# Kernel tuning notes

Hardware: AMD Instinct MI355X
Metric: run time of the kernel (lower is better)

The kernel has to match this reference:

```python
import jax, jax.numpy as jnp
import numpy as np

B, L, D, C, NL = 32, 512, 768, 97, 2  # batch, seq_len, hidden, class_nums, gat_layers


def setup_inputs() -> dict:
    key = jax.random.key(0)
    ks = jax.random.split(key, 16)

    def n(k, shape, scale=0.02):
        return jax.random.normal(k, shape, dtype=jnp.float32) * scale

    return dict(
        x=n(ks[0], (B, L, D), 1.0),                 # encoder output
        pos1=jnp.ones((B, L), jnp.float32),          # entity-1 position mask
        pos2=jnp.ones((B, L), jnp.float32),          # entity-2 position mask
        mask=jnp.ones((B, L), jnp.int32),            # attention mask (1 = keep)
        emb=n(ks[1], (C, D), 1.0),                   # relation label embedding table
        rel_w=n(ks[2], (D, D)), rel_b=jnp.zeros((D,), jnp.float32),
        # per-layer, per-RA (axis1: 0=ra1, 1=ra2) parameters
        qw=n(ks[3], (NL, 2, D, D)), qb=jnp.zeros((NL, 2, D), jnp.float32),
        kw=n(ks[4], (NL, 2, D, D)), kb=jnp.zeros((NL, 2, D), jnp.float32),
        vw=n(ks[5], (NL, 2, D, D)), vb=jnp.zeros((NL, 2, D), jnp.float32),
        sw=n(ks[6], (NL, 2, 2 * D)), sb=jnp.zeros((NL, 2), jnp.float32),   # score: Linear(2d,1)
        gw=n(ks[7], (NL, 2, 2 * D)), gb=jnp.zeros((NL, 2), jnp.float32),   # gate:  Linear(2d,1)
        fc1_w=n(ks[8], (3 * D, D)), fc1_b=jnp.zeros((D,), jnp.float32),
        fc2_w=n(ks[9], (D,)), fc2_b=jnp.zeros((), jnp.float32),
    )


def _relation_attention(p, x, qw, qb, kw, kb, vw, vb, sw, sb, gw, gb, mask):
    # p: (b, c, d) queries; x: (b, l, d) keys/values
    d = p.shape[-1]
    q = jnp.einsum('bcd,de->bce', p, qw) + qb          # (b, c, d)
    k = jnp.einsum('bld,de->ble', x, kw) + kb          # (b, l, d)
    # score = Linear(concat([q_i, k_j])) is separable: q@sw[:d] + k@sw[d:] + sb
    score = (q @ sw[:d])[:, :, None] + (k @ sw[d:])[:, None, :] + sb  # (b, c, l)
    if mask is not None:
        score = jnp.where(mask[:, None, :] == 0, jnp.float32(-1e9), score)
    attn = jax.nn.softmax(score, axis=2)
    v = jnp.einsum('bld,de->ble', x, vw) + vb          # (b, l, d)
    out = jnp.einsum('bcl,bld->bcd', attn, v) + p      # (b, c, d)
    # gate = sigmoid(Linear(concat([out, p]))), also separable
    g = jax.nn.sigmoid(out @ gw[:d] + p @ gw[d:] + gb)[..., None]
    return g * out + (1.0 - g) * p


def reference(x, pos1, pos2, mask, emb, rel_w, rel_b,
              qw, qb, kw, kb, vw, vb, sw, sb, gw, gb,
              fc1_w, fc1_b, fc2_w, fc2_b):
    b, d = x.shape[0], x.shape[-1]
    # p = relation(embedding(arange(C))) broadcast over batch
    p = emb @ rel_w + rel_b                            # (C, d)
    p = jnp.broadcast_to(p[None], (b,) + p.shape)      # (b, C, d)

    for li in range(qw.shape[0]):
        x = _relation_attention(x, p, qw[li, 0], qb[li, 0], kw[li, 0], kb[li, 0],
                                vw[li, 0], vb[li, 0], sw[li, 0], sb[li, 0],
                                gw[li, 0], gb[li, 0], None) + x
        p = _relation_attention(p, x, qw[li, 1], qb[li, 1], kw[li, 1], kb[li, 1],
                                vw[li, 1], vb[li, 1], sw[li, 1], sb[li, 1],
                                gw[li, 1], gb[li, 1], mask) + p

    def pool_avg(pos):
        return jnp.sum(x * pos[:, :, None], axis=1) / jnp.sum(pos, axis=1)[:, None]

    e1 = pool_avg(pos1)                                # (b, d)
    e2 = pool_avg(pos2)                                # (b, d)
    cshape = p.shape                                   # (b, C, d)
    pc = jnp.concatenate([p,
                          jnp.broadcast_to(e1[:, None, :], cshape),
                          jnp.broadcast_to(e2[:, None, :], cshape)], axis=2)  # (b, C, 3d)
    h = jnp.tanh(pc @ fc1_w + fc1_b)                   # (b, C, d)
    logits = jax.nn.sigmoid(h @ fc2_w + fc2_b)         # (b, C)
    pred = jnp.argmax(logits, axis=1)                  # (b,)
    return logits, pred
```

## Files before the change

### kernel.cpp

```cpp
#include <hip/hip_runtime.h>
#include <math.h>

#define NBLK 512
#define NTHR 256
static const int Bb = 32, Ls = 512, Dd = 768, Cc = 97;

struct KArgs {
    const float *x0, *pos1, *pos2;
    const int* mask;
    const float *emb, *rel_w, *rel_b, *kw, *vw, *vb, *sw, *gw, *gb;
    const float *fc1w, *fc1b, *fc2w, *fc2b;
    float* out;
    float *p0b, *pp, *sc, *avx1, *avx2, *av1, *av2, *aw1, *aw2, *S0, *S1, *xp1, *xp2, *geb;
    float *kvecs, *pdots, *g1buf, *xd;
    float* zbase;
    int zcount;
};

__device__ __forceinline__ float sigm(float x) { return 1.f / (1.f + expf(-x)); }

__device__ __forceinline__ float wred(float v) {
#pragma unroll
    for (int o = 32; o > 0; o >>= 1) v += __shfl_down(v, o, 64);
    return v;
}

__device__ __forceinline__ float blk_sum4(float v, float* shr) {
    v = wred(v);
    int t = threadIdx.x;
    if ((t & 63) == 0) shr[t >> 6] = v;
    __syncthreads();
    float r = shr[0] + shr[1] + shr[2] + shr[3];
    __syncthreads();
    return r;
}

__device__ void sgemm_direct(const float* __restrict__ A, const float* __restrict__ W,
                             const float* __restrict__ bias, float* __restrict__ C,
                             int M, int N, int K, int bx, int by,
                             float* As, float* Ws) {
    int tid = threadIdx.x;
    int tx = tid & 15, ty = tid >> 4;
    int bn = bx * 64, bm = by * 64;
    int arow = tid >> 2, akq = (tid & 3) << 2;
    int wrow = tid >> 4, wcol = (tid & 15) << 2;
    int gar = bm + arow;
    bool aval = gar < M;
    const float* Ap = A + (size_t)gar * K + akq;
    const float* Wp = W + (size_t)wrow * N + bn + wcol;
    float acc[4][4] = {{0.f}};
    float4 a4 = make_float4(0.f, 0.f, 0.f, 0.f);
    if (aval) a4 = *(const float4*)Ap;
    float4 w4 = *(const float4*)Wp;
    for (int k0 = 0; k0 < K; k0 += 16) {
        __syncthreads();
        As[(akq + 0) * 64 + arow] = a4.x; As[(akq + 1) * 64 + arow] = a4.y;
        As[(akq + 2) * 64 + arow] = a4.z; As[(akq + 3) * 64 + arow] = a4.w;
        *(float4*)&Ws[wrow * 64 + wcol] = w4;
        __syncthreads();
        if (k0 + 16 < K) {
            if (aval) a4 = *(const float4*)(Ap + k0 + 16);
            w4 = *(const float4*)(Wp + (size_t)(k0 + 16) * N);
        }
#pragma unroll
        for (int kk = 0; kk < 16; ++kk) {
            float4 a = *(const float4*)&As[kk * 64 + (ty << 2)];
            float4 b = *(const float4*)&Ws[kk * 64 + (tx << 2)];
            acc[0][0]+=a.x*b.x; acc[0][1]+=a.x*b.y; acc[0][2]+=a.x*b.z; acc[0][3]+=a.x*b.w;
            acc[1][0]+=a.y*b.x; acc[1][1]+=a.y*b.y; acc[1][2]+=a.y*b.z; acc[1][3]+=a.y*b.w;
            acc[2][0]+=a.z*b.x; acc[2][1]+=a.z*b.y; acc[2][2]+=a.z*b.z; acc[2][3]+=a.z*b.w;
            acc[3][0]+=a.w*b.x; acc[3][1]+=a.w*b.y; acc[3][2]+=a.w*b.z; acc[3][3]+=a.w*b.w;
        }
    }
    int gc = bn + (tx << 2);
    float4 bz4 = make_float4(0.f, 0.f, 0.f, 0.f);
    if (bias) bz4 = *(const float4*)(bias + gc);
#pragma unroll
    for (int i = 0; i < 4; ++i) {
        int gr = bm + (ty << 2) + i;
        if (gr < M) {
            float4 o = make_float4(acc[i][0] + bz4.x, acc[i][1] + bz4.y,
                                   acc[i][2] + bz4.z, acc[i][3] + bz4.w);
            *(float4*)(C + (size_t)gr * N + gc) = o;
        }
    }
}

__device__ void sm_w(const KArgs& a, int phase, int b, float* shr,
                     float& w0o, float& w1o, float& ga0, float& ga1,
                     float& gb0o, float& gb1o) {
    int t = threadIdx.x;
    float ks[2], ga[2], gb2[2] = {0.f, 0.f};
#pragma unroll
    for (int i = 0; i < 2; ++i) {
        int l = t + (i << 8);
        size_t r = (size_t)b * Ls + l;
        const float* px = a.xd + r * 4;
        float gp = sigm(px[0] + a.sc[b] + a.gb[0]);
        if (phase == 0) {
            ga[i] = gp;
            ks[i] = 2.f * px[1] + gp * a.sc[32 + b];
        } else {
            float g = sigm(2.f * px[2] + gp * a.sc[64 + b] + a.sc[224 + b] + a.gb[2]);
            ga[i] = gp; gb2[i] = g;
            ks[i] = 4.f * px[3] + 2.f * gp * a.sc[96 + b] + g * a.sc[256 + b];
        }
        if (a.mask[r] == 0) ks[i] = -1e9f;
    }
    float mx = fmaxf(ks[0], ks[1]);
#pragma unroll
    for (int o = 32; o > 0; o >>= 1) mx = fmaxf(mx, __shfl_down(mx, o, 64));
    if ((t & 63) == 0) shr[t >> 6] = mx;
    __syncthreads();
    mx = fmaxf(fmaxf(shr[0], shr[1]), fmaxf(shr[2], shr[3]));
    __syncthreads();
    float e0 = expf(ks[0] - mx), e1 = expf(ks[1] - mx);
    float s = blk_sum4(e0 + e1, shr);
    float inv = 1.f / s;
    w0o = e0 * inv; w1o = e1 * inv;
    ga0 = ga[0]; ga1 = ga[1];
    gb0o = gb2[0]; gb1o = gb2[1];
}

__device__ void coeff0_dev(const KArgs& a, int b, float* shr) {
    float w0, w1, ga0, ga1, u0, u1;
    sm_w(a, 0, b, shr, w0, w1, ga0, ga1, u0, u1);
    float ca = blk_sum4(w0 * ga0 + w1 * ga1, shr);
    if (threadIdx.x == 0) a.sc[320 + b] = ca;
}

__device__ void coeff1_dev(const KArgs& a, int b, float* shr) {
    int t = threadIdx.x;
    float w0, w1, ga0, ga1, g0, g1;
    sm_w(a, 1, b, shr, w0, w1, ga0, ga1, g0, g1);
    float ca = blk_sum4(w0 * ga0 + w1 * ga1, shr);
    if (t == 0) a.sc[352 + b] = ca;
    float cb = blk_sum4(w0 * g0 + w1 * g1, shr);
    if (t == 0) a.sc[384 + b] = cb;
    float q1a = a.pos1[(size_t)b * Ls + t], q1b = a.pos1[(size_t)b * Ls + t + 256];
    float q2a = a.pos2[(size_t)b * Ls + t], q2b = a.pos2[(size_t)b * Ls + t + 256];
    float s1 = blk_sum4(q1a + q1b, shr);
    float s2 = blk_sum4(q2a + q2b, shr);
    float c11 = blk_sum4(q1a * ga0 + q1b * ga1, shr);
    float c12 = blk_sum4(q1a * g0 + q1b * g1, shr);
    float c21 = blk_sum4(q2a * ga0 + q2b * ga1, shr);
    float c22 = blk_sum4(q2a * g0 + q2b * g1, shr);
    if (t == 0) {
        a.sc[448 + b] = c11; a.sc[480 + b] = c12;
        a.sc[512 + b] = c21; a.sc[544 + b] = c22;
        a.sc[576 + b] = 1.f / s1; a.sc[608 + b] = 1.f / s2;
    }
}

__device__ void attn_gemv(const KArgs& a, int phase, int jlin,
                          float* xs, float* lw, float* shr) {
    int t = threadIdx.x;
    int jt = jlin % 3, b = (jlin / 3) % 32, kseg = jlin / 96;
    float v = -3.0e38f, g1 = 0.f;
    if (t < Cc) {
        if (phase == 0) v = a.pdots[t];
        else {
            g1 = sigm(a.pdots[194 + t] + a.sc[128 + b] + a.gb[1]);
            v = 2.f * a.pdots[97 + t] + g1 * a.sc[160 + b];
        }
    }
    if (phase == 1 && jt == 0 && kseg == 0 && t < Cc) a.g1buf[(size_t)b * Cc + t] = g1;
    float m = v;
#pragma unroll
    for (int o = 32; o > 0; o >>= 1) m = fmaxf(m, __shfl_down(m, o, 64));
    if ((t & 63) == 0) shr[t >> 6] = m;
    __syncthreads();
    m = fmaxf(fmaxf(shr[0], shr[1]), fmaxf(shr[2], shr[3]));
    __syncthreads();
    float e = (t < Cc) ? expf(v - m) : 0.f;
    float s = blk_sum4(e, shr);
    float wc = e / s;
    if (t < Cc) lw[t] = wc;
    float cg1 = blk_sum4(wc * g1, shr);
    float alpha = (phase == 0) ? 1.f : 2.f;
    if (t < 96) {
        int d = kseg * 96 + t;
        const float* pc = a.p0b + d;
        float acc2 = 0.f;
#pragma unroll 4
        for (int c = 0; c < Cc; ++c) acc2 += lw[c] * pc[(size_t)c * Dd];
        float val = alpha * acc2;
        if (phase == 1) val += cg1 * a.av1[(size_t)b * Dd + d];
        xs[t] = val;
    }
    __syncthreads();
    const float* W = a.vw + (size_t)(phase == 0 ? 0 : 2) * Dd * Dd;
    const float* bias = a.vb + (phase == 0 ? 0 : 2) * Dd;
    float* outp = (phase == 0) ? a.avx1 : a.avx2;
    int j = jt * 256 + t;
    float acc = (kseg == 0) ? bias[j] : 0.f;
    const float* wp = W + (size_t)(kseg * 96) * Dd + j;
#pragma unroll 8
    for (int dd = 0; dd < 96; ++dd) acc += xs[dd] * wp[(size_t)dd * Dd];
    atomicAdd(&outp[(size_t)b * Dd + j], acc);
    const float* da[4]; const float* db[4]; int nd; float* dout;
    if (phase == 0) {
        da[0]=a.gw;          db[0]=nullptr;
        da[1]=a.kvecs+Dd;    db[1]=nullptr;
        da[2]=a.gw+3072;     db[2]=a.gw+3840;
        da[3]=a.kvecs+3*Dd;  db[3]=nullptr;
        nd = 4; dout = a.sc;
    } else {
        da[0]=a.gw+3072;     db[0]=nullptr;
        da[1]=a.kvecs+3*Dd;  db[1]=nullptr;
        nd = 2; dout = a.sc + 224;
    }
    for (int vv = 0; vv < nd; ++vv) {
        float wv = da[vv][j] + (db[vv] ? db[vv][j] : 0.f);
        float p = blk_sum4(acc * wv, shr);
        if (t == 0) atomicAdd(&dout[vv * 32 + b], p);
    }
    __syncthreads();
}

__device__ void mm_dev(const KArgs& a, int jlin, const float* S, float gamma,
                       const float* avA, const float* coefA, float multA,
                       const float* avB, const float* coefB, float multB,
                       const float* W, const float* bias, float* outp,
                       int ndots, const float* d0a, const float* d0b,
                       const float* d1a, const float* d2a, const float* d2b,
                       float* dout, float* xs, float* shr) {
    int t = threadIdx.x;
    int jt = jlin % 3, b = (jlin / 3) % 32, kseg = jlin / 96;
    if (t < 96) {
        int d = kseg * 96 + t;
        float v = gamma * S[(size_t)b * Dd + d];
        if (avA) v += multA * coefA[b] * avA[(size_t)b * Dd + d];
        if (avB) v += multB * coefB[b] * avB[(size_t)b * Dd + d];
        xs[t] = v;
    }
    __syncthreads();
    int j = jt * 256 + t;
    float acc = (kseg == 0 && bias) ? bias[j] : 0.f;
    const float* wp = W + (size_t)(kseg * 96) * Dd + j;
#pragma unroll 8
    for (int dd = 0; dd < 96; ++dd) acc += xs[dd] * wp[(size_t)dd * Dd];
    atomicAdd(&outp[(size_t)b * Dd + j], acc);
    if (ndots > 0) {
        float wv = d0a[j] + (d0b ? d0b[j] : 0.f);
        float p = blk_sum4(acc * wv, shr);
        if (t == 0) atomicAdd(&dout[b], p);
    }
    if (ndots > 1) {
        float p = blk_sum4(acc * d1a[j], shr);
        if (t == 0) atomicAdd(&dout[32 + b], p);
    }
    if (ndots > 2) {
        float wv = d2a[j] + (d2b ? d2b[j] : 0.f);
        float p = blk_sum4(acc * wv, shr);
        if (t == 0) atomicAdd(&dout[64 + b], p);
    }
}

__device__ void ge_dev(const KArgs& a, int jlin, float* xs, float* xs2) {
    int t = threadIdx.x;
    int jt = jlin % 3, b = (jlin / 3) % 32, kseg = jlin / 96;
    if (t < 96) {
        int d = kseg * 96 + t;
        float a1 = a.avx1[(size_t)b * Dd + d], a2 = a.avx2[(size_t)b * Dd + d];
        xs[t]  = (4.f * a.xp1[(size_t)b * Dd + d] + 2.f * a.sc[448 + b] * a1
                  + a.sc[480 + b] * a2) * a.sc[576 + b];
        xs2[t] = (4.f * a.xp2[(size_t)b * Dd + d] + 2.f * a.sc[512 + b] * a1
                  + a.sc[544 + b] * a2) * a.sc[608 + b];
    }
    __syncthreads();
    int j = jt * 256 + t;
    float a1 = 0.f, a2 = 0.f;
    const float* w1 = a.fc1w + (size_t)(Dd + kseg * 96) * Dd + j;
    const float* w2 = a.fc1w + (size_t)(2 * Dd + kseg * 96) * Dd + j;
#pragma unroll 8
    for (int dd = 0; dd < 96; ++dd) {
        a1 += xs[dd] * w1[(size_t)dd * Dd];
        a2 += xs2[dd] * w2[(size_t)dd * Dd];
    }
    float res = a1 + a2 + (kseg == 0 ? a.fc1b[j] : 0.f);
    atomicAdd(&a.geb[(size_t)b * Dd + j], res);
}

__device__ void aw_one(const KArgs& a, int jlin, const float* av, float* outp, float* xs) {
    int t = threadIdx.x;
    int jt = jlin % 3, b = (jlin / 3) % 32, kseg = jlin / 96;
    if (t < 96) xs[t] = av[(size_t)b * Dd + kseg * 96 + t];
    __syncthreads();
    int j = jt * 256 + t;
    float acc = 0.f;
    const float* wp = a.fc1w + (size_t)(kseg * 96) * Dd + j;
#pragma unroll 8
    for (int dd = 0; dd < 96; ++dd) acc += xs[dd] * wp[(size_t)dd * Dd];
    atomicAdd(&outp[(size_t)b * Dd + j], acc);
}

__device__ void passX_dev(const KArgs& a, int phase, int blk, float* S, bool dopos,
                          float* smw, float* shr) {
    int t = threadIdx.x;
    int b = blk >> 4, seg = blk & 15, l0 = seg * 32;
    {
        float w0, w1, u0, u1, u2, u3;
        sm_w(a, phase, b, shr, w0, w1, u0, u1, u2, u3);
        smw[t] = w0; smw[t + 256] = w1;
    }
    __syncthreads();
    if (t < 192) {
        int d4 = t << 2;
        const float* xb = a.x0 + ((size_t)b * Ls + l0) * Dd + d4;
        float4 as = make_float4(0.f,0.f,0.f,0.f);
        float4 a1 = make_float4(0.f,0.f,0.f,0.f);
        float4 a2 = make_float4(0.f,0.f,0.f,0.f);
        for (int l = 0; l < 32; ++l) {
            float4 xv = *(const float4*)(xb + (size_t)l * Dd);
            float wv = smw[l0 + l];
            as.x += wv*xv.x; as.y += wv*xv.y; as.z += wv*xv.z; as.w += wv*xv.w;
            if (dopos) {
                float q1 = a.pos1[(size_t)b * Ls + l0 + l], q2 = a.pos2[(size_t)b * Ls + l0 + l];
                a1.x += q1*xv.x; a1.y += q1*xv.y; a1.z += q1*xv.z; a1.w += q1*xv.w;
                a2.x += q2*xv.x; a2.y += q2*xv.y; a2.z += q2*xv.z; a2.w += q2*xv.w;
            }
        }
        float* ds = S + (size_t)b * Dd + d4;
        atomicAdd(ds+0, as.x); atomicAdd(ds+1, as.y); atomicAdd(ds+2, as.z); atomicAdd(ds+3, as.w);
        if (dopos) {
            float* d1 = a.xp1 + (size_t)b * Dd + d4;
            float* d2 = a.xp2 + (size_t)b * Dd + d4;
            atomicAdd(d1+0, a1.x); atomicAdd(d1+1, a1.y); atomicAdd(d1+2, a1.z); atomicAdd(d1+3, a1.w);
            atomicAdd(d2+0, a2.x); atomicAdd(d2+1, a2.y); atomicAdd(d2+2, a2.z); atomicAdd(d2+3, a2.w);
        }
    }
}

__device__ void kvec_dot(const KArgs& a, int dot, int lane) {
    int idx = dot / Dd, d = dot - idx * Dd;
    const float* row = a.kw + ((size_t)idx * Dd + d) * Dd;
    const float* swk = a.sw + (size_t)idx * 2 * Dd + Dd;
    float sA = 0.f;
    for (int j = lane; j < Dd; j += 64) sA += row[j] * swk[j];
    sA = wred(sA);
    if (lane == 0) a.kvecs[dot] = sA;
}

__device__ void xdots_dev(const KArgs& a, int r0, int rstep, int lane) {
    float4 gs0[3], k1r[3], gs2[3], k3r[3];
#pragma unroll
    for (int k = 0; k < 3; ++k) {
        int d = (lane << 2) + k * 256;
        float4 ga = *(const float4*)(a.gw + d);
        float4 gbv = *(const float4*)(a.gw + 768 + d);
        gs0[k] = make_float4(ga.x+gbv.x, ga.y+gbv.y, ga.z+gbv.z, ga.w+gbv.w);
        k1r[k] = *(const float4*)(a.kvecs + 768 + d);
        float4 g2a = *(const float4*)(a.gw + 3072 + d);
        float4 g2b = *(const float4*)(a.gw + 3840 + d);
        gs2[k] = make_float4(g2a.x+g2b.x, g2a.y+g2b.y, g2a.z+g2b.z, g2a.w+g2b.w);
        k3r[k] = *(const float4*)(a.kvecs + 2304 + d);
    }
    for (int r = r0; r < Bb * Ls; r += rstep) {
        const float* xr = a.x0 + (size_t)r * Dd;
        float s0 = 0.f, s1 = 0.f, s2 = 0.f, s3 = 0.f;
#pragma unroll
        for (int k = 0; k < 3; ++k) {
            float4 xv = *(const float4*)(xr + (lane << 2) + k * 256);
            s0 += xv.x*gs0[k].x + xv.y*gs0[k].y + xv.z*gs0[k].z + xv.w*gs0[k].w;
            s1 += xv.x*k1r[k].x + xv.y*k1r[k].y + xv.z*k1r[k].z + xv.w*k1r[k].w;
            s2 += xv.x*gs2[k].x + xv.y*gs2[k].y + xv.z*gs2[k].z + xv.w*gs2[k].w;
            s3 += xv.x*k3r[k].x + xv.y*k3r[k].y + xv.z*k3r[k].z + xv.w*k3r[k].w;
        }
        s0 = wred(s0); s1 = wred(s1); s2 = wred(s2); s3 = wred(s3);
        if (lane == 0) {
            float4 o4 = make_float4(s0, s1, s2, s3);
            *(float4*)(a.xd + (size_t)r * 4) = o4;
        }
    }
}

__device__ void pdots_dev(const KArgs& a, int g2, int lane) {
    for (int k = 0; k < 4; ++k) {
        int j = g2 + k * 128;
        if (k == 3) { if (g2 >= 4) break; j = 384 + g2; }
        if (j >= 388) continue;
        int vv = j / Cc, r = j - vv * Cc;
        const float* va; const float* vb2 = nullptr;
        if (vv == 0) va = a.kvecs;
        else if (vv == 1) va = a.kvecs + 2 * Dd;
        else if (vv == 2) { va = a.gw + 1536; vb2 = a.gw + 2304; }
        else { va = a.gw + 4608; vb2 = a.gw + 5376; }
        const float* row = a.p0b + (size_t)r * Dd;
        float sA = 0.f;
        for (int jj = lane; jj < Dd; jj += 64)
            sA += row[jj] * (va[jj] + (vb2 ? vb2[jj] : 0.f));
        sA = wred(sA);
        if (lane == 0) a.pdots[j] = sA;
    }
}

__device__ void logits_dev(const KArgs& a, int r, float* shr) {
    int t = threadIdx.x;
    int b = r / Cc, c = r - b * Cc;
    float g1 = a.g1buf[r];
    float g2 = sigm(2.f * a.pdots[291 + c] + g1 * a.sc[192 + b] + a.sc[288 + b] + a.gb[3]);
    float ssum = 0.f;
#pragma unroll
    for (int sseg = 0; sseg < 3; ++sseg) {
        int d = t + sseg * 256;
        float h = tanhf(4.f * a.pp[(size_t)c * Dd + d]
                      + 2.f * g1 * a.aw1[(size_t)b * Dd + d]
                      + g2 * a.aw2[(size_t)b * Dd + d]
                      + a.geb[(size_t)b * Dd + d]);
        ssum += h * a.fc2w[d];
    }
    float tt = blk_sum4(ssum, shr);
    if (t == 0) a.out[r] = sigm(tt + a.fc2b[0]);
}

__global__ __launch_bounds__(NTHR) void k_zg(KArgs a) {
    __shared__ float As[1024], Ws[1024];
    int blk = blockIdx.x, t = threadIdx.x;
    int wv_ = t >> 6, lane = t & 63;
    if (blk < 24) {
        sgemm_direct(a.emb, a.rel_w, a.rel_b, a.p0b, Cc, Dd, Dd, blk % 12, blk / 12, As, Ws);
    } else {
        for (size_t i = (size_t)(blk - 24) * NTHR + t; i < (size_t)a.zcount;
             i += (size_t)(NBLK - 24) * NTHR)
            a.zbase[i] = 0.f;
        for (int dot = (blk - 24) * 4 + wv_; dot < 3072; dot += (NBLK - 24) * 4)
            kvec_dot(a, dot, lane);
    }
}

__global__ __launch_bounds__(NTHR) void k_prep2(KArgs a) {
    __shared__ float As[1024], Ws[1024];
    int blk = blockIdx.x, t = threadIdx.x;
    int wv_ = t >> 6, lane = t & 63;
    if (blk < 24) {
        sgemm_direct(a.p0b, a.fc1w, nullptr, a.pp, Cc, Dd, Dd, blk % 12, blk / 12, As, Ws);
    } else if (blk < 56) {
        pdots_dev(a, (blk - 24) * 4 + wv_, lane);
    } else {
        xdots_dev(a, (blk - 56) * 4 + wv_, (NBLK - 56) * 4, lane);
    }
}

__global__ __launch_bounds__(NTHR) void k_attn0(KArgs a) {
    __shared__ float xs[96], lw[128], shr[16];
    attn_gemv(a, 0, blockIdx.x, xs, lw, shr);
}

__global__ __launch_bounds__(NTHR) void k_p3(KArgs a) {
    __shared__ float smw[512], shr[16];
    int blk = blockIdx.x;
    if (blk < 512) passX_dev(a, 0, blk, a.S0, true, smw, shr);
    else coeff0_dev(a, blk - 512, shr);
}

__global__ __launch_bounds__(NTHR) void k_mm0(KArgs a) {
    __shared__ float xs[96], shr[16];
    mm_dev(a, blockIdx.x, a.S0, 2.f, a.avx1, a.sc + 320, 1.f, nullptr, nullptr, 0.f,
           a.vw + (size_t)1 * Dd * Dd, a.vb + Dd, a.av1,
           3, a.gw + 1536, nullptr, a.kvecs + 2 * Dd, a.gw + 4608, a.gw + 5376,
           a.sc + 128, xs, shr);
}

__global__ __launch_bounds__(NTHR) void k_p5(KArgs a) {
    __shared__ float xs[96], lw[128], shr[16];
    int blk = blockIdx.x;
    if (blk < 768) attn_gemv(a, 1, blk, xs, lw, shr);
    else aw_one(a, blk - 768, a.av1, a.aw1, xs);
}

__global__ __launch_bounds__(NTHR) void k_p6(KArgs a) {
    __shared__ float smw[512], shr[16];
    int blk = blockIdx.x;
    if (blk < 512) passX_dev(a, 1, blk, a.S1, false, smw, shr);
    else coeff1_dev(a, blk - 512, shr);
}

__global__ __launch_bounds__(NTHR) void k_p7(KArgs a) {
    __shared__ float xs[96], xs2[96], shr[16];
    int blk = blockIdx.x;
    if (blk < 768)
        mm_dev(a, blk, a.S1, 4.f, a.avx1, a.sc + 352, 2.f, a.avx2, a.sc + 384, 1.f,
               a.vw + (size_t)3 * Dd * Dd, a.vb + 3 * Dd, a.av2,
               1, a.gw + 4608, nullptr, nullptr, nullptr, nullptr,
               a.sc + 288, xs, shr);
    else ge_dev(a, blk - 768, xs, xs2);
}

__global__ __launch_bounds__(NTHR) void k_aw2(KArgs a) {
    __shared__ float xs[96];
    aw_one(a, blockIdx.x, a.av2, a.aw2, xs);
}

__global__ __launch_bounds__(NTHR) void k_logits(KArgs a) {
    __shared__ float shr[16];
    for (int r = blockIdx.x; r < Bb * Cc; r += NBLK) logits_dev(a, r, shr);
}

__global__ void k_argmax(KArgs a) {
    int t = threadIdx.x;
    if (t < Bb) {
        const float* row = a.out + (size_t)t * Cc;
        float best = row[0];
        int bi = 0;
        for (int c = 1; c < Cc; ++c) {
            float v = row[c];
            if (v > best) { best = v; bi = c; }
        }
        a.out[Bb * Cc + t] = (float)bi;
    }
}

extern "C" void kernel_launch(void* const* d_in, const int* in_sizes, int n_in,
                              void* d_out, int out_size, void* d_ws, size_t ws_size,
                              hipStream_t stream) {
    KArgs ka;
    ka.x0    = (const float*)d_in[0];
    ka.pos1  = (const float*)d_in[1];
    ka.pos2  = (const float*)d_in[2];
    ka.mask  = (const int*)d_in[3];
    ka.emb   = (const float*)d_in[4];
    ka.rel_w = (const float*)d_in[5];
    ka.rel_b = (const float*)d_in[6];
    ka.kw    = (const float*)d_in[9];
    ka.vw    = (const float*)d_in[11];
    ka.vb    = (const float*)d_in[12];
    ka.sw    = (const float*)d_in[13];
    ka.gw    = (const float*)d_in[15];
    ka.gb    = (const float*)d_in[16];
    ka.fc1w  = (const float*)d_in[17];
    ka.fc1b  = (const float*)d_in[18];
    ka.fc2w  = (const float*)d_in[19];
    ka.fc2b  = (const float*)d_in[20];
    ka.out   = (float*)d_out;

    float* ws = (float*)d_ws;
    size_t off = 0;
    const size_t PD = (size_t)Cc * Dd;
    const size_t BD = (size_t)Bb * Dd;
    ka.p0b  = ws + off; off += PD;
    ka.pp   = ws + off; off += PD;
    size_t zstart = off;
    ka.sc   = ws + off; off += 640;
    ka.avx1 = ws + off; off += BD;
    ka.avx2 = ws + off; off += BD;
    ka.av1  = ws + off; off += BD;
    ka.av2  = ws + off; off += BD;
    ka.aw1  = ws + off; off += BD;
    ka.aw2  = ws + off; off += BD;
    ka.S0   = ws + off; off += BD;
    ka.S1   = ws + off; off += BD;
    ka.xp1  = ws + off; off += BD;
    ka.xp2  = ws + off; off += BD;
    ka.geb  = ws + off; off += BD;
    ka.zbase = ws + zstart;
    ka.zcount = (int)(off - zstart);
    ka.kvecs = ws + off; off += (size_t)4 * Dd;
    ka.pdots = ws + off; off += 388;
    ka.g1buf = ws + off; off += (size_t)Bb * Cc;
    ka.xd    = ws + off; off += (size_t)Bb * Ls * 4;

    k_zg<<<NBLK, NTHR, 0, stream>>>(ka);
    k_prep2<<<NBLK, NTHR, 0, stream>>>(ka);
    k_attn0<<<768, NTHR, 0, stream>>>(ka);
    k_p3<<<544, NTHR, 0, stream>>>(ka);
    k_mm0<<<768, NTHR, 0, stream>>>(ka);
    k_p5<<<1536, NTHR, 0, stream>>>(ka);
    k_p6<<<544, NTHR, 0, stream>>>(ka);
    k_p7<<<1536, NTHR, 0, stream>>>(ka);
    k_aw2<<<768, NTHR, 0, stream>>>(ka);
    k_logits<<<NBLK, NTHR, 0, stream>>>(ka);
    k_argmax<<<1, 64, 0, stream>>>(ka);
}
```

Measured before the change: 366.5 us.

## Split-K the two small GEMMs with atomic accumulation and memset zeroing

Result: faster. 329.6 us (-10.1%).

```diff
diff --git a/kernel.cpp b/kernel.cpp
--- a/kernel.cpp
+++ b/kernel.cpp
@@ -13,8 +13,6 @@
     float* out;
     float *p0b, *pp, *sc, *avx1, *avx2, *av1, *av2, *aw1, *aw2, *S0, *S1, *xp1, *xp2, *geb;
     float *kvecs, *pdots, *g1buf, *xd;
-    float* zbase;
-    int zcount;
 };
 
 __device__ __forceinline__ float sigm(float x) { return 1.f / (1.f + expf(-x)); }
@@ -35,30 +33,31 @@
     return r;
 }
 
-__device__ void sgemm_direct(const float* __restrict__ A, const float* __restrict__ W,
-                             const float* __restrict__ bias, float* __restrict__ C,
-                             int M, int N, int K, int bx, int by,
-                             float* As, float* Ws) {
+__device__ void sgemm_dev(const float* __restrict__ A, const float* __restrict__ W,
+                          const float* __restrict__ bias, float* __restrict__ C,
+                          int M, int N, int K, int KC, int bx, int by, int bz,
+                          float* As, float* Ws) {
     int tid = threadIdx.x;
     int tx = tid & 15, ty = tid >> 4;
     int bn = bx * 64, bm = by * 64;
+    int kb = bz * KC;
     int arow = tid >> 2, akq = (tid & 3) << 2;
     int wrow = tid >> 4, wcol = (tid & 15) << 2;
     int gar = bm + arow;
     bool aval = gar < M;
-    const float* Ap = A + (size_t)gar * K + akq;
-    const float* Wp = W + (size_t)wrow * N + bn + wcol;
+    const float* Ap = A + (size_t)gar * K + kb + akq;
+    const float* Wp = W + (size_t)(kb + wrow) * N + bn + wcol;
     float acc[4][4] = {{0.f}};
     float4 a4 = make_float4(0.f, 0.f, 0.f, 0.f);
     if (aval) a4 = *(const float4*)Ap;
     float4 w4 = *(const float4*)Wp;
-    for (int k0 = 0; k0 < K; k0 += 16) {
+    for (int k0 = 0; k0 < KC; k0 += 16) {
         __syncthreads();
         As[(akq + 0) * 64 + arow] = a4.x; As[(akq + 1) * 64 + arow] = a4.y;
         As[(akq + 2) * 64 + arow] = a4.z; As[(akq + 3) * 64 + arow] = a4.w;
         *(float4*)&Ws[wrow * 64 + wcol] = w4;
         __syncthreads();
-        if (k0 + 16 < K) {
+        if (k0 + 16 < KC) {
             if (aval) a4 = *(const float4*)(Ap + k0 + 16);
             w4 = *(const float4*)(Wp + (size_t)(k0 + 16) * N);
         }
@@ -74,14 +73,14 @@
     }
     int gc = bn + (tx << 2);
     float4 bz4 = make_float4(0.f, 0.f, 0.f, 0.f);
-    if (bias) bz4 = *(const float4*)(bias + gc);
+    if (bz == 0 && bias) bz4 = *(const float4*)(bias + gc);
 #pragma unroll
     for (int i = 0; i < 4; ++i) {
         int gr = bm + (ty << 2) + i;
         if (gr < M) {
-            float4 o = make_float4(acc[i][0] + bz4.x, acc[i][1] + bz4.y,
-                                   acc[i][2] + bz4.z, acc[i][3] + bz4.w);
-            *(float4*)(C + (size_t)gr * N + gc) = o;
+            float* cp = C + (size_t)gr * N + gc;
+            atomicAdd(cp + 0, acc[i][0] + bz4.x); atomicAdd(cp + 1, acc[i][1] + bz4.y);
+            atomicAdd(cp + 2, acc[i][2] + bz4.z); atomicAdd(cp + 3, acc[i][3] + bz4.w);
         }
     }
 }
@@ -414,17 +413,15 @@
     if (t == 0) a.out[r] = sigm(tt + a.fc2b[0]);
 }
 
-__global__ __launch_bounds__(NTHR) void k_zg(KArgs a) {
+__global__ __launch_bounds__(NTHR) void k_g1kv(KArgs a) {
     __shared__ float As[1024], Ws[1024];
     int blk = blockIdx.x, t = threadIdx.x;
     int wv_ = t >> 6, lane = t & 63;
-    if (blk < 24) {
-        sgemm_direct(a.emb, a.rel_w, a.rel_b, a.p0b, Cc, Dd, Dd, blk % 12, blk / 12, As, Ws);
+    if (blk < 192) {
+        sgemm_dev(a.emb, a.rel_w, a.rel_b, a.p0b, Cc, Dd, Dd, 96,
+                  blk % 12, (blk / 12) % 2, blk / 24, As, Ws);
     } else {
-        for (size_t i = (size_t)(blk - 24) * NTHR + t; i < (size_t)a.zcount;
-             i += (size_t)(NBLK - 24) * NTHR)
-            a.zbase[i] = 0.f;
-        for (int dot = (blk - 24) * 4 + wv_; dot < 3072; dot += (NBLK - 24) * 4)
+        for (int dot = (blk - 192) * 4 + wv_; dot < 3072; dot += (NBLK - 192) * 4)
             kvec_dot(a, dot, lane);
     }
 }
@@ -433,12 +430,13 @@
     __shared__ float As[1024], Ws[1024];
     int blk = blockIdx.x, t = threadIdx.x;
     int wv_ = t >> 6, lane = t & 63;
-    if (blk < 24) {
-        sgemm_direct(a.p0b, a.fc1w, nullptr, a.pp, Cc, Dd, Dd, blk % 12, blk / 12, As, Ws);
-    } else if (blk < 56) {
-        pdots_dev(a, (blk - 24) * 4 + wv_, lane);
+    if (blk < 96) {
+        sgemm_dev(a.p0b, a.fc1w, nullptr, a.pp, Cc, Dd, Dd, 192,
+                  blk % 12, (blk / 12) % 2, blk / 24, As, Ws);
+    } else if (blk < 128) {
+        pdots_dev(a, (blk - 96) * 4 + wv_, lane);
     } else {
-        xdots_dev(a, (blk - 56) * 4 + wv_, (NBLK - 56) * 4, lane);
+        xdots_dev(a, (blk - 128) * 4 + wv_, (NBLK - 128) * 4, lane);
     }
 }
 
@@ -540,7 +538,6 @@
     const size_t BD = (size_t)Bb * Dd;
     ka.p0b  = ws + off; off += PD;
     ka.pp   = ws + off; off += PD;
-    size_t zstart = off;
     ka.sc   = ws + off; off += 640;
     ka.avx1 = ws + off; off += BD;
     ka.avx2 = ws + off; off += BD;
@@ -553,14 +550,14 @@
     ka.xp1  = ws + off; off += BD;
     ka.xp2  = ws + off; off += BD;
     ka.geb  = ws + off; off += BD;
-    ka.zbase = ws + zstart;
-    ka.zcount = (int)(off - zstart);
+    size_t zbytes = off * sizeof(float);
     ka.kvecs = ws + off; off += (size_t)4 * Dd;
     ka.pdots = ws + off; off += 388;
     ka.g1buf = ws + off; off += (size_t)Bb * Cc;
     ka.xd    = ws + off; off += (size_t)Bb * Ls * 4;
 
-    k_zg<<<NBLK, NTHR, 0, stream>>>(ka);
+    hipMemsetAsync((void*)ws, 0, zbytes, stream);
+    k_g1kv<<<NBLK, NTHR, 0, stream>>>(ka);
     k_prep2<<<NBLK, NTHR, 0, stream>>>(ka);
     k_attn0<<<768, NTHR, 0, stream>>>(ka);
     k_p3<<<544, NTHR, 0, stream>>>(ka);
```
